# Performance work log

Measured on AMD Instinct MI355X. Metric: run time of the kernel, lower is better.

## Reference

```python
import jax, jax.numpy as jnp
import numpy as np

EMBED_DIM = 1024
NUM_HEADS = 16
HEAD_DIM = EMBED_DIM // NUM_HEADS
MAX_DIST = 128
NUM_BUCKETS = 2 * MAX_DIST + 1  # 257: fixes off-by-one in original Embedding sizing


def setup_inputs() -> dict:
    key = jax.random.key(0)
    ks = jax.random.split(key, 10)
    B, S, D = 2, 2048, EMBED_DIM
    s = 1.0 / np.sqrt(D)
    return {
        "x": jax.random.normal(ks[0], (B, S, D), dtype=jnp.float32),
        "Wq": jax.random.normal(ks[1], (D, D), dtype=jnp.float32) * s,
        "bq": jnp.zeros((D,), dtype=jnp.float32),
        "Wk": jax.random.normal(ks[2], (D, D), dtype=jnp.float32) * s,
        "bk": jnp.zeros((D,), dtype=jnp.float32),
        "Wv": jax.random.normal(ks[3], (D, D), dtype=jnp.float32) * s,
        "bv": jnp.zeros((D,), dtype=jnp.float32),
        "Wo": jax.random.normal(ks[4], (D, D), dtype=jnp.float32) * s,
        "bo": jnp.zeros((D,), dtype=jnp.float32),
        "rel_emb": jax.random.normal(ks[5], (NUM_BUCKETS, NUM_HEADS), dtype=jnp.float32) * 0.02,
    }


def _rel_bias(rel_emb, seq_len):
    # relative position clamped to [-MAX_DIST, MAX_DIST], shifted to [0, 2*MAX_DIST]
    pos = jnp.arange(seq_len)
    rel = jnp.clip(pos[:, None] - pos[None, :], -MAX_DIST, MAX_DIST) + MAX_DIST
    bias = rel_emb[rel]                    # [S, S, H]
    return jnp.transpose(bias, (2, 0, 1))  # [H, S, S]


def reference(x, Wq, bq, Wk, bk, Wv, bv, Wo, bo, rel_emb):
    B, S, D = x.shape
    H, Hd = NUM_HEADS, HEAD_DIM
    # torch Linear: y = x @ W.T + b
    q = (x @ Wq.T + bq).reshape(B, S, H, Hd).transpose(0, 2, 1, 3)  # [B,H,S,Hd]
    k = (x @ Wk.T + bk).reshape(B, S, H, Hd).transpose(0, 2, 1, 3)
    v = (x @ Wv.T + bv).reshape(B, S, H, Hd).transpose(0, 2, 1, 3)
    scores = jnp.einsum("bhqd,bhkd->bhqk", q, k) / jnp.sqrt(jnp.float32(Hd))
    scores = scores + _rel_bias(rel_emb, S)[None]  # add [H,S,S] bias
    probs = jax.nn.softmax(scores, axis=-1)
    out = jnp.einsum("bhqk,bhkd->bhqd", probs, v)
    out = out.transpose(0, 2, 1, 3).reshape(B, S, D)
    return out @ Wo.T + bo
```

## Files before the change

### kernel.cpp

```cpp
#include <hip/hip_runtime.h>
#include <hip/hip_bf16.h>
#include <cstdint>
#include <cstddef>

#define DEVI __device__ __forceinline__

static constexpr int SEQ = 2048;
static constexpr int DM  = 1024;
static constexpr int NH  = 16;
static constexpr int HD  = 64;
static constexpr int NTOK = 2 * SEQ;
static constexpr int NBUCKET = 257;
static constexpr float LOG2E = 1.44269504088896f;

typedef __attribute__((ext_vector_type(8))) short bf16x8;
typedef __attribute__((ext_vector_type(4))) float f32x4;
#define MFMA16(a, b, c) __builtin_amdgcn_mfma_f32_16x16x32_bf16((a), (b), (c), 0, 0, 0)

DEVI float bf1(uint16_t u)  { return __uint_as_float(((uint32_t)u) << 16); }
DEVI uint16_t f2bf(float f) {
    uint32_t x = __float_as_uint(f);
    x += 0x7fffu + ((x >> 16) & 1u);
    return (uint16_t)(x >> 16);
}
DEVI bf16x8 ld_frag(const uint16_t* p) {
    union { uint4 u; bf16x8 f; } c;
    c.u = *(const uint4*)p;
    return c.f;
}
DEVI void gld16(const uint16_t* g, uint16_t* l) {
    __builtin_amdgcn_global_load_lds(
        (const __attribute__((address_space(1))) uint32_t*)g,
        (__attribute__((address_space(3))) uint32_t*)l, 16, 0, 0);
}

__global__ void sniff_kernel(const uint16_t* __restrict__ x, int* __restrict__ flag)
{
    int bad = 0;
    for (int i = threadIdx.x; i < 512; i += 64) {
        const float v = bf1(x[i]);
        if (!(fabsf(v) < 64.0f)) bad = 1;
    }
    const unsigned long long m = __ballot(bad);
    if (threadIdx.x == 0) *flag = (m != 0ull) ? 1 : 0;
}

__global__ __launch_bounds__(256)
void convert_kernel(const void* __restrict__ x, const void* __restrict__ Wq,
                    const void* __restrict__ Wk, const void* __restrict__ Wv,
                    const void* __restrict__ Wo, const void* __restrict__ bq,
                    const void* __restrict__ bk, const void* __restrict__ bv,
                    const void* __restrict__ bo, uint16_t* __restrict__ dst,
                    const int* __restrict__ flagp)
{
    const bool f32in = (*flagp != 0);
    const size_t M4 = 4194304, M1 = 1048576;
    const size_t e = ((size_t)blockIdx.x * 256 + threadIdx.x) * 8;
    const void* src; size_t off;
    if      (e < M4)                 { src = x;  off = e; }
    else if (e < M4 + M1)            { src = Wq; off = e - M4; }
    else if (e < M4 + 2*M1)          { src = Wk; off = e - M4 - M1; }
    else if (e < M4 + 3*M1)          { src = Wv; off = e - M4 - 2*M1; }
    else if (e < M4 + 4*M1)          { src = Wo; off = e - M4 - 3*M1; }
    else if (e < M4 + 4*M1 + 1024)   { src = bq; off = e - M4 - 4*M1; }
    else if (e < M4 + 4*M1 + 2048)   { src = bk; off = e - M4 - 4*M1 - 1024; }
    else if (e < M4 + 4*M1 + 3072)   { src = bv; off = e - M4 - 4*M1 - 2048; }
    else                             { src = bo; off = e - M4 - 4*M1 - 3072; }
    if (f32in) {
        const float4 a = *(const float4*)((const float*)src + off);
        const float4 b = *(const float4*)((const float*)src + off + 4);
        uint4 o;
        o.x = (uint32_t)f2bf(a.x) | ((uint32_t)f2bf(a.y) << 16);
        o.y = (uint32_t)f2bf(a.z) | ((uint32_t)f2bf(a.w) << 16);
        o.z = (uint32_t)f2bf(b.x) | ((uint32_t)f2bf(b.y) << 16);
        o.w = (uint32_t)f2bf(b.z) | ((uint32_t)f2bf(b.w) << 16);
        *(uint4*)(dst + e) = o;
    } else {
        *(uint4*)(dst + e) = *(const uint4*)((const uint16_t*)src + off);
    }
}

__global__ __launch_bounds__(256)
void gemm_qkv(const uint16_t* __restrict__ xc, const uint16_t* __restrict__ Wqkv,
              const uint16_t* __restrict__ bqkv,
              uint16_t* __restrict__ Qw, uint16_t* __restrict__ Kw,
              uint16_t* __restrict__ Vt)
{
    __shared__ uint16_t As[128 * 32];
    __shared__ uint16_t Bs[128 * 32];
    const int tid = threadIdx.x, bx = blockIdx.x;
    const int lane = tid & 63, wave = tid >> 6;
    const int ln = lane & 15, quad = lane >> 4;
    const int wm = (wave & 1) * 64, wn = (wave >> 1) * 64;

    const uint16_t *Ab, *Bb;
    int bm, bn, vor;
    if (bx < 512) {
        vor = 0; bm = (bx >> 4) * 128; bn = (bx & 15) * 128;
        Ab = xc + (size_t)bm * DM;  Bb = Wqkv + (size_t)bn * DM;
    } else {
        vor = 1; const int b2 = bx - 512; bm = (b2 >> 5) * 128; bn = (b2 & 31) * 128;
        Ab = Wqkv + (size_t)(2048 + bm) * DM;  Bb = xc + (size_t)bn * DM;
    }

    f32x4 acc[4][4];
    #pragma unroll
    for (int i = 0; i < 4; ++i)
        #pragma unroll
        for (int j = 0; j < 4; ++j) acc[i][j] = (f32x4){0.f, 0.f, 0.f, 0.f};

    const int s0 = tid, s1 = 256 + tid;
    const uint16_t* ga0 = Ab + (size_t)(s0 >> 2) * DM + (s0 & 3) * 8;
    const uint16_t* ga1 = Ab + (size_t)(s1 >> 2) * DM + (s1 & 3) * 8;
    const uint16_t* gb0 = Bb + (size_t)(s0 >> 2) * DM + (s0 & 3) * 8;
    const uint16_t* gb1 = Bb + (size_t)(s1 >> 2) * DM + (s1 & 3) * 8;

    for (int k0 = 0; k0 < DM; k0 += 32) {
        __syncthreads();
        gld16(ga0 + k0, &As[s0 * 8]);
        gld16(ga1 + k0, &As[s1 * 8]);
        gld16(gb0 + k0, &Bs[s0 * 8]);
        gld16(gb1 + k0, &Bs[s1 * 8]);
        __syncthreads();

        bf16x8 af[4], bfr[4];
        #pragma unroll
        for (int t = 0; t < 4; ++t) {
            af[t]  = ld_frag(&As[(wm + t * 16 + ln) * 32 + quad * 8]);
            bfr[t] = ld_frag(&Bs[(wn + t * 16 + ln) * 32 + quad * 8]);
        }
        #pragma unroll
        for (int ti = 0; ti < 4; ++ti)
            #pragma unroll
            for (int tj = 0; tj < 4; ++tj)
                acc[ti][tj] = MFMA16(af[ti], bfr[tj], acc[ti][tj]);
    }

    if (!vor) {
        #pragma unroll
        for (int tj = 0; tj < 4; ++tj) {
            const int c = bn + wn + tj * 16 + ln;
            const int mat = c >> 10, h = (c >> 6) & 15, hd = c & 63;
            uint16_t* dstp = mat ? Kw : Qw;
            const float scale = mat ? 1.0f : (0.125f * LOG2E);
            const float bb = bf1(bqkv[c]);
            #pragma unroll
            for (int ti = 0; ti < 4; ++ti)
                #pragma unroll
                for (int r = 0; r < 4; ++r) {
                    const int row = bm + wm + ti * 16 + quad * 4 + r;
                    const int b = row >> 11, s = row & 2047;
                    dstp[(((size_t)b * NH + h) * SEQ + s) * HD + hd] =
                        f2bf((acc[ti][tj][r] + bb) * scale);
                }
        }
    } else {
        #pragma unroll
        for (int ti = 0; ti < 4; ++ti)
            #pragma unroll
            for (int r = 0; r < 4; ++r) {
                const int f = bm + wm + ti * 16 + quad * 4 + r;
                const int h = f >> 6, hd = f & 63;
                const float bb = bf1(bqkv[2048 + f]);
                #pragma unroll
                for (int tj = 0; tj < 4; ++tj) {
                    const int t = bn + wn + tj * 16 + ln;
                    const int b = t >> 11, s = t & 2047;
                    Vt[(((size_t)b * NH + h) * HD + hd) * SEQ + s] = f2bf(acc[ti][tj][r] + bb);
                }
            }
    }
}

__global__ __launch_bounds__(256)
void gemm_out(const uint16_t* __restrict__ Cw, const uint16_t* __restrict__ Woc,
              const uint16_t* __restrict__ boc, void* __restrict__ out,
              const int* __restrict__ flagp)
{
    __shared__ uint16_t As[128 * 32];
    __shared__ uint16_t Bs[64 * 32];
    const int tid = threadIdx.x, bx = blockIdx.x;
    const int lane = tid & 63, wave = tid >> 6;
    const int ln = lane & 15, quad = lane >> 4;
    const int wm = (wave & 1) * 64, wn = (wave >> 1) * 32;
    const int bm = (bx >> 4) * 128, bn = (bx & 15) * 64;
    const uint16_t* Ab = Cw + (size_t)bm * DM;
    const uint16_t* Bb = Woc + (size_t)bn * DM;

    f32x4 acc[4][2];
    #pragma unroll
    for (int i = 0; i < 4; ++i)
        #pragma unroll
        for (int j = 0; j < 2; ++j) acc[i][j] = (f32x4){0.f, 0.f, 0.f, 0.f};

    const int s0 = tid, s1 = 256 + tid;
    const uint16_t* ga0 = Ab + (size_t)(s0 >> 2) * DM + (s0 & 3) * 8;
    const uint16_t* ga1 = Ab + (size_t)(s1 >> 2) * DM + (s1 & 3) * 8;
    const uint16_t* gb0 = Bb + (size_t)(s0 >> 2) * DM + (s0 & 3) * 8;

    for (int k0 = 0; k0 < DM; k0 += 32) {
        __syncthreads();
        gld16(ga0 + k0, &As[s0 * 8]);
        gld16(ga1 + k0, &As[s1 * 8]);
        gld16(gb0 + k0, &Bs[s0 * 8]);
        __syncthreads();

        bf16x8 af[4], bfr[2];
        #pragma unroll
        for (int t = 0; t < 4; ++t)
            af[t] = ld_frag(&As[(wm + t * 16 + ln) * 32 + quad * 8]);
        #pragma unroll
        for (int t = 0; t < 2; ++t)
            bfr[t] = ld_frag(&Bs[(wn + t * 16 + ln) * 32 + quad * 8]);
        #pragma unroll
        for (int ti = 0; ti < 4; ++ti)
            #pragma unroll
            for (int tj = 0; tj < 2; ++tj)
                acc[ti][tj] = MFMA16(af[ti], bfr[tj], acc[ti][tj]);
    }

    const bool f32o = (*flagp != 0);
    #pragma unroll
    for (int tj = 0; tj < 2; ++tj) {
        const int c = bn + wn + tj * 16 + ln;
        const float bb = bf1(boc[c]);
        #pragma unroll
        for (int ti = 0; ti < 4; ++ti)
            #pragma unroll
            for (int r = 0; r < 4; ++r) {
                const int row = bm + wm + ti * 16 + quad * 4 + r;
                const float v = acc[ti][tj][r] + bb;
                if (f32o) ((float*)out)[(size_t)row * DM + c] = v;
                else      ((uint16_t*)out)[(size_t)row * DM + c] = f2bf(v);
            }
    }
}

#define ATTN_COMPUTE(K0, KSB, VSB)                                             \
  do {                                                                         \
    const int mode_ = ((K0) >= q0 + 256) ? 0 : (((K0) + 192 <= q0) ? 2 : 1);   \
    if (mode_ != 1) {                                                          \
      const float binit_ = (mode_ == 0) ? bneg : bpos;                         \
      _Pragma("unroll")                                                        \
      for (int nt = 0; nt < 4; ++nt) {                                         \
        const bf16x8 kf0 = ld_frag((KSB) + kvo[nt][0]);                        \
        const bf16x8 kf1 = ld_frag((KSB) + kvo[nt][1]);                        \
        _Pragma("unroll")                                                      \
        for (int qg = 0; qg < 2; ++qg) {                                       \
          f32x4 s4 = (f32x4){binit_, binit_, binit_, binit_};                  \
          s4 = MFMA16(kf0, qf0[qg], s4);                                       \
          s4 = MFMA16(kf1, qf1[qg], s4);                                       \
          uint32_t pb[4];                                                      \
          _Pragma("unroll")                                                    \
          for (int r = 0; r < 4; ++r)                                          \
            pb[r] = __float_as_uint(__builtin_amdgcn_exp2f(s4[r]));            \
          const uint2 dw = {__builtin_amdgcn_perm(pb[1], pb[0], 0x07060302u),  \
                            __builtin_amdgcn_perm(pb[3], pb[2], 0x07060302u)}; \
          *(uint2*)Pw[qg][nt] = dw;                                            \
        }                                                                      \
      }                                                                        \
    } else {                                                                   \
      _Pragma("unroll")                                                        \
      for (int nt = 0; nt < 4; ++nt) {                                         \
        const bf16x8 kf0 = ld_frag((KSB) + kvo[nt][0]);                        \
        const bf16x8 kf1 = ld_frag((KSB) + kvo[nt][1]);                        \
        _Pragma("unroll")                                                      \
        for (int qg = 0; qg < 2; ++qg) {                                       \
          const int iq_ = q0 + wave * 32 + qg * 16 + ln + 128 - (K0) - quad * 4;\
          f32x4 s4 = (f32x4){0.f, 0.f, 0.f, 0.f};                              \
          s4 = MFMA16(kf0, qf0[qg], s4);                                       \
          s4 = MFMA16(kf1, qf1[qg], s4);                                       \
          uint32_t pb[4];                                                      \
          _Pragma("unroll")                                                    \
          for (int r = 0; r < 4; ++r) {                                        \
            int x_ = iq_ - (nt * 16 + r);                                      \
            x_ = max(0, min(256, x_));                                         \
            pb[r] = __float_as_uint(__builtin_amdgcn_exp2f(s4[r] + bias_s[x_]));\
          }                                                                    \
          const uint2 dw = {__builtin_amdgcn_perm(pb[1], pb[0], 0x07060302u),  \
                            __builtin_amdgcn_perm(pb[3], pb[2], 0x07060302u)}; \
          *(uint2*)Pw[qg][nt] = dw;                                            \
        }                                                                      \
      }                                                                        \
    }                                                                          \
    bf16x8 pfa[2], pfb[2];                                                     \
    _Pragma("unroll")                                                          \
    for (int qg = 0; qg < 2; ++qg) {                                           \
      pfa[qg] = ld_frag(pfp[qg][0]);                                           \
      pfb[qg] = ld_frag(pfp[qg][1]);                                           \
      lf[qg] = MFMA16(pfa[qg], onef, lf[qg]);                                  \
      lf[qg] = MFMA16(pfb[qg], onef, lf[qg]);                                  \
    }                                                                          \
    _Pragma("unroll")                                                          \
    for (int dt = 0; dt < 4; ++dt) {                                           \
      const bf16x8 vfa = ld_frag((VSB) + kvo[dt][0]);                          \
      const bf16x8 vfb = ld_frag((VSB) + kvo[dt][1]);                          \
      _Pragma("unroll")                                                        \
      for (int qg = 0; qg < 2; ++qg) {                                         \
        o[qg][dt] = MFMA16(pfa[qg], vfa, o[qg][dt]);                           \
        o[qg][dt] = MFMA16(pfb[qg], vfb, o[qg][dt]);                           \
      }                                                                        \
    }                                                                          \
  } while (0)

__global__ __launch_bounds__(256, 2)
void attn_mfma(const uint16_t* __restrict__ Q, const uint16_t* __restrict__ K,
               const uint16_t* __restrict__ Vt, const void* __restrict__ rel,
               uint16_t* __restrict__ ctx, const int* __restrict__ flagp)
{
    __shared__ alignas(16) uint16_t Ks[2][64 * 64];
    __shared__ alignas(16) uint16_t Vls[2][64 * 64];
    __shared__ alignas(16) uint16_t Pl[4][32 * 64];
    __shared__ float bias_s[NBUCKET];

    const bool f32in = (*flagp != 0);
    const int tid = threadIdx.x, wave = tid >> 6, lane = tid & 63;
    const int ln = lane & 15, quad = lane >> 4;

    const int blk = blockIdx.x;
    const int bh = (blk & 7) * 4 + ((blk >> 3) & 3);
    const int qt = blk >> 5;
    const int b = bh >> 4, h = bh & 15;
    const int q0 = qt * 128;

    const float C8 = 8.0f * LOG2E;
    for (int i = tid; i < NBUCKET; i += 256) {
        const float bv = f32in ? ((const float*)rel)[i * NH + h]
                               : bf1(((const uint16_t*)rel)[i * NH + h]);
        bias_s[i] = bv * LOG2E - C8;
    }

    bf16x8 qf0[2], qf1[2];
    #pragma unroll
    for (int qg = 0; qg < 2; ++qg) {
        const uint16_t* qp =
            Q + ((size_t)bh * SEQ + q0 + wave * 32 + qg * 16 + ln) * HD;
        qf0[qg] = ld_frag(qp + quad * 8);
        qf1[qg] = ld_frag(qp + 32 + quad * 8);
    }

    union { uint4 u; bf16x8 f; } onec;
    onec.u = (uint4){0x3F803F80u, 0x3F803F80u, 0x3F803F80u, 0x3F803F80u};
    const bf16x8 onef = onec.f;

    f32x4 o[2][4];
    f32x4 lf[2];
    #pragma unroll
    for (int qg = 0; qg < 2; ++qg) {
        lf[qg] = (f32x4){0.f, 0.f, 0.f, 0.f};
        #pragma unroll
        for (int dt = 0; dt < 4; ++dt) o[qg][dt] = (f32x4){0.f, 0.f, 0.f, 0.f};
    }

    const int swz = ln & 7;
    uint16_t* myP = Pl[wave];

    const int s0_ = tid, s1_ = tid + 256;
    const int r0_ = s0_ >> 3, c0_ = (s0_ & 7) ^ (r0_ & 7);
    const int r1_ = s1_ >> 3, c1_ = (s1_ & 7) ^ (r1_ & 7);
    const int koff0 = r0_ * HD + c0_ * 8,  koff1 = r1_ * HD + c1_ * 8;
    const int voff0 = r0_ * SEQ + c0_ * 8, voff1 = r1_ * SEQ + c1_ * 8;
    uint16_t* const kd00 = &Ks[0][s0_ * 8];
    uint16_t* const kd01 = &Ks[0][s1_ * 8];
    uint16_t* const kd10 = &Ks[1][s0_ * 8];
    uint16_t* const kd11 = &Ks[1][s1_ * 8];
    uint16_t* const vd00 = &Vls[0][s0_ * 8];
    uint16_t* const vd01 = &Vls[0][s1_ * 8];
    uint16_t* const vd10 = &Vls[1][s0_ * 8];
    uint16_t* const vd11 = &Vls[1][s1_ * 8];

    const uint16_t* kg = K  + (size_t)bh * SEQ * HD;
    const uint16_t* vg = Vt + (size_t)bh * HD * SEQ;

    int kvo[4][2];
    #pragma unroll
    for (int t = 0; t < 4; ++t) {
        const int row = (t * 16 + ln) * 64;
        kvo[t][0] = row + ((0 + quad) ^ swz) * 8;
        kvo[t][1] = row + ((4 + quad) ^ swz) * 8;
    }
    uint16_t* Pw[2][4];
    const uint16_t* pfp[2][2];
    #pragma unroll
    for (int qg = 0; qg < 2; ++qg) {
        const int prow = (qg * 16 + ln) * 64;
        #pragma unroll
        for (int nt = 0; nt < 4; ++nt) {
            const int cb = (2 * nt + (quad >> 1)) ^ swz;
            Pw[qg][nt] = &myP[prow + cb * 8 + (quad & 1) * 4];
        }
        pfp[qg][0] = &myP[prow + ((0 + quad) ^ swz) * 8];
        pfp[qg][1] = &myP[prow + ((4 + quad) ^ swz) * 8];
    }

    gld16(kg + koff0, kd00); gld16(kg + koff1, kd01);
    gld16(vg + voff0, vd00); gld16(vg + voff1, vd01);
    kg += 64 * HD; vg += 64;
    __syncthreads();
    const float bneg = bias_s[0], bpos = bias_s[256];

    for (int t = 0; t < 16; ++t) {
        gld16(kg + koff0, kd10); gld16(kg + koff1, kd11);
        gld16(vg + voff0, vd10); gld16(vg + voff1, vd11);
        kg += 64 * HD; vg += 64;
        ATTN_COMPUTE(t * 128, &Ks[0][0], &Vls[0][0]);
        __syncthreads();

        if (t < 15) {
            gld16(kg + koff0, kd00); gld16(kg + koff1, kd01);
            gld16(vg + voff0, vd00); gld16(vg + voff1, vd01);
            kg += 64 * HD; vg += 64;
        }
        ATTN_COMPUTE(t * 128 + 64, &Ks[1][0], &Vls[1][0]);
        __syncthreads();
    }

    #pragma unroll
    for (int qg = 0; qg < 2; ++qg)
        #pragma unroll
        for (int r = 0; r < 4; ++r) {
            const float inv = 1.0f / lf[qg][r];
            const int qq = q0 + wave * 32 + qg * 16 + quad * 4 + r;
            #pragma unroll
            for (int dt = 0; dt < 4; ++dt)
                ctx[(((size_t)b * SEQ + qq) * NH + h) * HD + dt * 16 + ln] =
                    f2bf(o[qg][dt][r] * inv);
        }
}

extern "C" void kernel_launch(void* const* d_in, const int* in_sizes, int n_in,
                              void* d_out, int out_size, void* d_ws, size_t ws_size,
                              hipStream_t stream)
{
    const void* x   = d_in[0];
    const void* Wq  = d_in[1];
    const void* bq  = d_in[2];
    const void* Wk  = d_in[3];
    const void* bk  = d_in[4];
    const void* Wv  = d_in[5];
    const void* bv  = d_in[6];
    const void* Wo  = d_in[7];
    const void* bo  = d_in[8];
    const void* rel = d_in[9];

    const size_t M4 = 4194304, M1 = 1048576;
    uint16_t* ws16 = (uint16_t*)d_ws;
    uint16_t* xc   = ws16;
    uint16_t* Wqkv = ws16 + M4;
    uint16_t* Woc  = ws16 + M4 + 3 * M1;
    uint16_t* bqkv = ws16 + M4 + 4 * M1;
    uint16_t* boc  = bqkv + 3072;
    uint16_t* Qw   = ws16 + M4 + 4 * M1 + 8192;
    uint16_t* Kw   = Qw + M4;
    uint16_t* Vt   = Kw + M4;
    int* flag = (int*)(Vt + M4);
    uint16_t* Cw = xc;

    sniff_kernel<<<1, 64, 0, stream>>>((const uint16_t*)x, flag);
    convert_kernel<<<4098, 256, 0, stream>>>(x, Wq, Wk, Wv, Wo, bq, bk, bv, bo,
                                             ws16, flag);
    gemm_qkv<<<768, 256, 0, stream>>>(xc, Wqkv, bqkv, Qw, Kw, Vt);
    attn_mfma<<<512, 256, 0, stream>>>(Qw, Kw, Vt, rel, Cw, flag);
    gemm_out<<<512, 256, 0, stream>>>(Cw, Woc, boc, d_out, flag);
}
```

Before: 205.7 us.

## Switch attention to 32x32 MFMA and keep P in registers via lane shuffles

The attention inner loop moves from 16x16x32 MFMA tiles to 32x32x16 tiles, with S^T accumulated so the probability matrix can be repacked in registers. Cross-half-wave shuffles replace the per-wave P round trip through LDS, so the P shared buffer and its stores and reloads are removed. The exp now runs on full f32x16 accumulators and the bias-free/bias-constant modes share one path. The risk is higher register pressure from 16-wide accumulators and preloaded K/V fragments, plus the cost of the shuffles.

```diff
diff --git a/kernel.cpp b/kernel.cpp
--- a/kernel.cpp
+++ b/kernel.cpp
@@ -15,7 +15,9 @@
 
 typedef __attribute__((ext_vector_type(8))) short bf16x8;
 typedef __attribute__((ext_vector_type(4))) float f32x4;
+typedef __attribute__((ext_vector_type(16))) float f32x16;
 #define MFMA16(a, b, c) __builtin_amdgcn_mfma_f32_16x16x32_bf16((a), (b), (c), 0, 0, 0)
+#define MFMA32(a, b, c) __builtin_amdgcn_mfma_f32_32x32x16_bf16((a), (b), (c), 0, 0, 0)
 
 DEVI float bf1(uint16_t u)  { return __uint_as_float(((uint32_t)u) << 16); }
 DEVI uint16_t f2bf(float f) {
@@ -33,6 +35,7 @@
         (const __attribute__((address_space(1))) uint32_t*)g,
         (__attribute__((address_space(3))) uint32_t*)l, 16, 0, 0);
 }
+DEVI uint32_t xsw32(uint32_t v) { return (uint32_t)__shfl_xor((int)v, 32, 64); }
 
 __global__ void sniff_kernel(const uint16_t* __restrict__ x, int* __restrict__ flag)
 {
@@ -236,70 +239,79 @@
     }
 }
 
+#define PK2(a, b) ((uint32_t)f2bf(a) | ((uint32_t)f2bf(b) << 16))
+
+#define P_BUILD(SA, PA_LO, PA_HI)                                              \
+  do {                                                                         \
+    const uint32_t c0_ = PK2((SA)[0], (SA)[1]);                                \
+    const uint32_t c1_ = PK2((SA)[2], (SA)[3]);                                \
+    const uint32_t c2_ = PK2((SA)[4], (SA)[5]);                                \
+    const uint32_t c3_ = PK2((SA)[6], (SA)[7]);                                \
+    const uint32_t c4_ = PK2((SA)[8], (SA)[9]);                                \
+    const uint32_t c5_ = PK2((SA)[10], (SA)[11]);                              \
+    const uint32_t c6_ = PK2((SA)[12], (SA)[13]);                              \
+    const uint32_t c7_ = PK2((SA)[14], (SA)[15]);                              \
+    const uint32_t p0_ = xsw32(c0_), p1_ = xsw32(c1_);                         \
+    const uint32_t p2_ = xsw32(c2_), p3_ = xsw32(c3_);                         \
+    const uint32_t p4_ = xsw32(c4_), p5_ = xsw32(c5_);                         \
+    const uint32_t p6_ = xsw32(c6_), p7_ = xsw32(c7_);                         \
+    union { uint32_t u[4]; bf16x8 f; } lo_, hi_;                               \
+    lo_.u[0] = hi ? p2_ : c0_;  lo_.u[1] = hi ? p3_ : c1_;                     \
+    lo_.u[2] = hi ? c2_ : p0_;  lo_.u[3] = hi ? c3_ : p1_;                     \
+    hi_.u[0] = hi ? p6_ : c4_;  hi_.u[1] = hi ? p7_ : c5_;                     \
+    hi_.u[2] = hi ? c6_ : p4_;  hi_.u[3] = hi ? c7_ : p5_;                     \
+    (PA_LO) = lo_.f; (PA_HI) = hi_.f;                                          \
+  } while (0)
+
 #define ATTN_COMPUTE(K0, KSB, VSB)                                             \
   do {                                                                         \
     const int mode_ = ((K0) >= q0 + 256) ? 0 : (((K0) + 192 <= q0) ? 2 : 1);   \
-    if (mode_ != 1) {                                                          \
-      const float binit_ = (mode_ == 0) ? bneg : bpos;                         \
+    bf16x8 kf_[2][4], vf_[2][4];                                               \
+    _Pragma("unroll")                                                          \
+    for (int kb = 0; kb < 2; ++kb)                                             \
       _Pragma("unroll")                                                        \
-      for (int nt = 0; nt < 4; ++nt) {                                         \
-        const bf16x8 kf0 = ld_frag((KSB) + kvo[nt][0]);                        \
-        const bf16x8 kf1 = ld_frag((KSB) + kvo[nt][1]);                        \
-        _Pragma("unroll")                                                      \
-        for (int qg = 0; qg < 2; ++qg) {                                       \
-          f32x4 s4 = (f32x4){binit_, binit_, binit_, binit_};                  \
-          s4 = MFMA16(kf0, qf0[qg], s4);                                       \
-          s4 = MFMA16(kf1, qf1[qg], s4);                                       \
-          uint32_t pb[4];                                                      \
-          _Pragma("unroll")                                                    \
-          for (int r = 0; r < 4; ++r)                                          \
-            pb[r] = __float_as_uint(__builtin_amdgcn_exp2f(s4[r]));            \
-          const uint2 dw = {__builtin_amdgcn_perm(pb[1], pb[0], 0x07060302u),  \
-                            __builtin_amdgcn_perm(pb[3], pb[2], 0x07060302u)}; \
-          *(uint2*)Pw[qg][nt] = dw;                                            \
-        }                                                                      \
-      }                                                                        \
-    } else {                                                                   \
+      for (int ds = 0; ds < 4; ++ds)                                           \
+        kf_[kb][ds] = ld_frag((KSB) + kfo[kb][ds]);                            \
+    _Pragma("unroll")                                                          \
+    for (int db = 0; db < 2; ++db)                                             \
       _Pragma("unroll")                                                        \
-      for (int nt = 0; nt < 4; ++nt) {                                         \
-        const bf16x8 kf0 = ld_frag((KSB) + kvo[nt][0]);                        \
-        const bf16x8 kf1 = ld_frag((KSB) + kvo[nt][1]);                        \
-        _Pragma("unroll")                                                      \
-        for (int qg = 0; qg < 2; ++qg) {                                       \
-          const int iq_ = q0 + wave * 32 + qg * 16 + ln + 128 - (K0) - quad * 4;\
-          f32x4 s4 = (f32x4){0.f, 0.f, 0.f, 0.f};                              \
-          s4 = MFMA16(kf0, qf0[qg], s4);                                       \
-          s4 = MFMA16(kf1, qf1[qg], s4);                                       \
-          uint32_t pb[4];                                                      \
-          _Pragma("unroll")                                                    \
-          for (int r = 0; r < 4; ++r) {                                        \
-            int x_ = iq_ - (nt * 16 + r);                                      \
-            x_ = max(0, min(256, x_));                                         \
-            pb[r] = __float_as_uint(__builtin_amdgcn_exp2f(s4[r] + bias_s[x_]));\
-          }                                                                    \
-          const uint2 dw = {__builtin_amdgcn_perm(pb[1], pb[0], 0x07060302u),  \
-                            __builtin_amdgcn_perm(pb[3], pb[2], 0x07060302u)}; \
-          *(uint2*)Pw[qg][nt] = dw;                                            \
-        }                                                                      \
+      for (int kc = 0; kc < 4; ++kc)                                           \
+        vf_[db][kc] = ld_frag((VSB) + vfo[db][kc]);                            \
+    f32x16 sa0, sa1;                                                           \
+    {                                                                          \
+      const float binit_ = (mode_ == 0) ? bneg : ((mode_ == 2) ? bpos : 0.f);  \
+      _Pragma("unroll")                                                        \
+      for (int r = 0; r < 16; ++r) { sa0[r] = binit_; sa1[r] = binit_; }       \
+    }                                                                          \
+    _Pragma("unroll")                                                          \
+    for (int ds = 0; ds < 4; ++ds) {                                           \
+      sa0 = MFMA32(kf_[0][ds], qb[ds], sa0);                                   \
+      sa1 = MFMA32(kf_[1][ds], qb[ds], sa1);                                   \
+    }                                                                          \
+    if (mode_ == 1) {                                                          \
+      const int iq0_ = q0 + wave * 32 + l31 + 128 - (K0) - 4 * hi;             \
+      _Pragma("unroll")                                                        \
+      for (int r = 0; r < 16; ++r) {                                           \
+        const int ko_ = (r & 3) + 8 * (r >> 2);                                \
+        const int x0_ = max(0, min(256, iq0_ - ko_));                          \
+        const int x1_ = max(0, min(256, iq0_ - 32 - ko_));                     \
+        sa0[r] += bias_s[x0_];                                                 \
+        sa1[r] += bias_s[x1_];                                                 \
       }                                                                        \
     }                                                                          \
-    bf16x8 pfa[2], pfb[2];                                                     \
     _Pragma("unroll")                                                          \
-    for (int qg = 0; qg < 2; ++qg) {                                           \
-      pfa[qg] = ld_frag(pfp[qg][0]);                                           \
-      pfb[qg] = ld_frag(pfp[qg][1]);                                           \
-      lf[qg] = MFMA16(pfa[qg], onef, lf[qg]);                                  \
-      lf[qg] = MFMA16(pfb[qg], onef, lf[qg]);                                  \
+    for (int r = 0; r < 16; ++r) {                                             \
+      sa0[r] = __builtin_amdgcn_exp2f(sa0[r]);                                 \
+      sa1[r] = __builtin_amdgcn_exp2f(sa1[r]);                                 \
     }                                                                          \
+    bf16x8 pa_[4];                                                             \
+    P_BUILD(sa0, pa_[0], pa_[1]);                                              \
+    P_BUILD(sa1, pa_[2], pa_[3]);                                              \
     _Pragma("unroll")                                                          \
-    for (int dt = 0; dt < 4; ++dt) {                                           \
-      const bf16x8 vfa = ld_frag((VSB) + kvo[dt][0]);                          \
-      const bf16x8 vfb = ld_frag((VSB) + kvo[dt][1]);                          \
-      _Pragma("unroll")                                                        \
-      for (int qg = 0; qg < 2; ++qg) {                                         \
-        o[qg][dt] = MFMA16(pfa[qg], vfa, o[qg][dt]);                           \
-        o[qg][dt] = MFMA16(pfb[qg], vfb, o[qg][dt]);                           \
-      }                                                                        \
+    for (int kc = 0; kc < 4; ++kc) {                                           \
+      lf    = MFMA32(pa_[kc], onef, lf);                                       \
+      o2[0] = MFMA32(pa_[kc], vf_[0][kc], o2[0]);                              \
+      o2[1] = MFMA32(pa_[kc], vf_[1][kc], o2[1]);                              \
     }                                                                          \
   } while (0)
 
@@ -310,12 +322,11 @@
 {
     __shared__ alignas(16) uint16_t Ks[2][64 * 64];
     __shared__ alignas(16) uint16_t Vls[2][64 * 64];
-    __shared__ alignas(16) uint16_t Pl[4][32 * 64];
     __shared__ float bias_s[NBUCKET];
 
     const bool f32in = (*flagp != 0);
     const int tid = threadIdx.x, wave = tid >> 6, lane = tid & 63;
-    const int ln = lane & 15, quad = lane >> 4;
+    const int l31 = lane & 31, hi = lane >> 5;
 
     const int blk = blockIdx.x;
     const int bh = (blk & 7) * 4 + ((blk >> 3) & 3);
@@ -330,36 +341,27 @@
         bias_s[i] = bv * LOG2E - C8;
     }
 
-    bf16x8 qf0[2], qf1[2];
-    #pragma unroll
-    for (int qg = 0; qg < 2; ++qg) {
-        const uint16_t* qp =
-            Q + ((size_t)bh * SEQ + q0 + wave * 32 + qg * 16 + ln) * HD;
-        qf0[qg] = ld_frag(qp + quad * 8);
-        qf1[qg] = ld_frag(qp + 32 + quad * 8);
+    bf16x8 qb[4];
+    {
+        const uint16_t* qp = Q + ((size_t)bh * SEQ + q0 + wave * 32 + l31) * HD;
+        #pragma unroll
+        for (int ds = 0; ds < 4; ++ds)
+            qb[ds] = ld_frag(qp + ds * 16 + hi * 8);
     }
 
     union { uint4 u; bf16x8 f; } onec;
     onec.u = (uint4){0x3F803F80u, 0x3F803F80u, 0x3F803F80u, 0x3F803F80u};
     const bf16x8 onef = onec.f;
 
-    f32x4 o[2][4];
-    f32x4 lf[2];
-    #pragma unroll
-    for (int qg = 0; qg < 2; ++qg) {
-        lf[qg] = (f32x4){0.f, 0.f, 0.f, 0.f};
-        #pragma unroll
-        for (int dt = 0; dt < 4; ++dt) o[qg][dt] = (f32x4){0.f, 0.f, 0.f, 0.f};
-    }
-
-    const int swz = ln & 7;
-    uint16_t* myP = Pl[wave];
+    f32x16 o2[2], lf;
+    #pragma unroll
+    for (int r = 0; r < 16; ++r) { o2[0][r] = 0.f; o2[1][r] = 0.f; lf[r] = 0.f; }
 
     const int s0_ = tid, s1_ = tid + 256;
-    const int r0_ = s0_ >> 3, c0_ = (s0_ & 7) ^ (r0_ & 7);
-    const int r1_ = s1_ >> 3, c1_ = (s1_ & 7) ^ (r1_ & 7);
-    const int koff0 = r0_ * HD + c0_ * 8,  koff1 = r1_ * HD + c1_ * 8;
-    const int voff0 = r0_ * SEQ + c0_ * 8, voff1 = r1_ * SEQ + c1_ * 8;
+    const int r0_ = s0_ >> 3, c0s_ = (s0_ & 7) ^ (r0_ & 7);
+    const int r1_ = s1_ >> 3, c1s_ = (s1_ & 7) ^ (r1_ & 7);
+    const int koff0 = r0_ * HD + c0s_ * 8,  koff1 = r1_ * HD + c1s_ * 8;
+    const int voff0 = r0_ * SEQ + c0s_ * 8, voff1 = r1_ * SEQ + c1s_ * 8;
     uint16_t* const kd00 = &Ks[0][s0_ * 8];
     uint16_t* const kd01 = &Ks[0][s1_ * 8];
     uint16_t* const kd10 = &Ks[1][s0_ * 8];
@@ -372,26 +374,18 @@
     const uint16_t* kg = K  + (size_t)bh * SEQ * HD;
     const uint16_t* vg = Vt + (size_t)bh * HD * SEQ;
 
-    int kvo[4][2];
-    #pragma unroll
-    for (int t = 0; t < 4; ++t) {
-        const int row = (t * 16 + ln) * 64;
-        kvo[t][0] = row + ((0 + quad) ^ swz) * 8;
-        kvo[t][1] = row + ((4 + quad) ^ swz) * 8;
-    }
-    uint16_t* Pw[2][4];
-    const uint16_t* pfp[2][2];
-    #pragma unroll
-    for (int qg = 0; qg < 2; ++qg) {
-        const int prow = (qg * 16 + ln) * 64;
-        #pragma unroll
-        for (int nt = 0; nt < 4; ++nt) {
-            const int cb = (2 * nt + (quad >> 1)) ^ swz;
-            Pw[qg][nt] = &myP[prow + cb * 8 + (quad & 1) * 4];
-        }
-        pfp[qg][0] = &myP[prow + ((0 + quad) ^ swz) * 8];
-        pfp[qg][1] = &myP[prow + ((4 + quad) ^ swz) * 8];
-    }
+    const int swz = l31 & 7;
+    int kfo[2][4], vfo[2][4];
+    #pragma unroll
+    for (int kb = 0; kb < 2; ++kb)
+        #pragma unroll
+        for (int ds = 0; ds < 4; ++ds)
+            kfo[kb][ds] = (kb * 32 + l31) * 64 + ((ds * 2 + hi) ^ swz) * 8;
+    #pragma unroll
+    for (int db = 0; db < 2; ++db)
+        #pragma unroll
+        for (int kc = 0; kc < 4; ++kc)
+            vfo[db][kc] = (db * 32 + l31) * 64 + ((kc * 2 + hi) ^ swz) * 8;
 
     gld16(kg + koff0, kd00); gld16(kg + koff1, kd01);
     gld16(vg + voff0, vd00); gld16(vg + voff1, vd01);
@@ -416,16 +410,14 @@
     }
 
     #pragma unroll
-    for (int qg = 0; qg < 2; ++qg)
-        #pragma unroll
-        for (int r = 0; r < 4; ++r) {
-            const float inv = 1.0f / lf[qg][r];
-            const int qq = q0 + wave * 32 + qg * 16 + quad * 4 + r;
-            #pragma unroll
-            for (int dt = 0; dt < 4; ++dt)
-                ctx[(((size_t)b * SEQ + qq) * NH + h) * HD + dt * 16 + ln] =
-                    f2bf(o[qg][dt][r] * inv);
-        }
+    for (int r = 0; r < 16; ++r) {
+        const float inv = 1.0f / lf[r];
+        const int qq = q0 + wave * 32 + (r & 3) + 8 * (r >> 2) + 4 * hi;
+        #pragma unroll
+        for (int db = 0; db < 2; ++db)
+            ctx[(((size_t)b * SEQ + qq) * NH + h) * HD + db * 32 + l31] =
+                f2bf(o2[db][r] * inv);
+    }
 }
 
 extern "C" void kernel_launch(void* const* d_in, const int* in_sizes, int n_in,
```

Measured after the change: 219.4 us. 1.07x slower.
